# Kernel tuning notes

Hardware: AMD Instinct MI355X
Metric: run time of the kernel (lower is better)

Reference implementation:

```python
import jax, jax.numpy as jnp
import numpy as np

EPS = 1e-5
N, DEG, D, L = 50000, 16, 128, 2  # nodes, max_neighbor, embed_size, gnn_layer


def _log_map_zero(y):
    # Poincare ball log map at origin: atanh(||y||) * y / ||y||, with clamps
    n = jnp.linalg.norm(y, axis=-1, keepdims=True)
    nc = jnp.clip(n, EPS, 1.0 - EPS)
    return y * (jnp.arctanh(nc) / nc)


def _exp_map_zero(v):
    # Poincare ball exp map at origin: tanh(||v||) * v / ||v||
    n = jnp.linalg.norm(v, axis=-1, keepdims=True)
    nc = jnp.maximum(n, EPS)
    return v * (jnp.tanh(nc) / nc)


def setup_inputs() -> dict:
    key = jax.random.key(0)
    k1, k2, k3, k4, k5 = jax.random.split(key, 5)
    node_repr = jax.random.normal(k1, (N, D), jnp.float32) * 0.1
    adj = jax.random.randint(k2, (N, DEG), 0, N)
    weight = jax.random.normal(k3, (N, DEG), jnp.float32)
    mask = jnp.ones((N, 1), jnp.float32)
    # per-relation, per-layer message weights (2 relations: pos / neg edges)
    scale = 1.0 / np.sqrt(D)
    W_pos = jax.random.normal(k4, (L, D, D), jnp.float32) * scale
    W_neg = jax.random.normal(k5, (L, D, D), jnp.float32) * scale
    return {"node_repr": node_repr, "adj": adj, "weight": weight,
            "mask": mask, "W_pos": W_pos, "W_neg": W_neg}


def reference(node_repr, adj, weight, mask, W_pos, W_neg):
    # split_graph_by_negative_edge
    pos_m = (weight > 0).astype(weight.dtype)
    neg_m = (weight < 0).astype(weight.dtype)
    adjs = (adj * pos_m.astype(adj.dtype), adj * neg_m.astype(adj.dtype))
    ws = (weight * pos_m, (-weight) * neg_m)
    Ws = (W_pos, W_neg)

    x = node_repr
    for step in range(L):
        x = (_log_map_zero(x) if step > 0 else x) * mask
        combined = jnp.zeros_like(x)
        for a, w, W in zip(adjs, ws, Ws):
            msg = (x @ W[step]) * mask                    # [N, D]
            nb = msg[a.reshape(-1)].reshape(N, DEG, D)    # neighbor gather
            combined = combined + jnp.sum(w[..., None] * nb, axis=1)
        combined = combined * mask                        # dropout identity (eval)
        x = _exp_map_zero(combined) * mask
        x = jax.nn.relu(x) * mask                         # poincare activation
    return x
```

## Files before the change

### kernel.cpp

```cpp
#include <hip/hip_runtime.h>
#include <math.h>

#define DD 128
#define DEG 16
#define TM 16
#define LDST 136
#define EPSV 1e-5f

typedef _Float16 half4_t __attribute__((ext_vector_type(4)));
typedef _Float16 half8_t __attribute__((ext_vector_type(8)));
typedef float    f32x4   __attribute__((ext_vector_type(4)));

__global__ void prep_x(const float* __restrict__ x, const float* __restrict__ mask,
                       _Float16* __restrict__ x16, int n4)
{
    int i = blockIdx.x * blockDim.x + threadIdx.x;
    if (i >= n4) return;
    float m = mask[i >> 5];
    float m2 = m * m;
    float4 v = ((const float4*)x)[i];
    half4_t h;
    h[0] = (_Float16)(v.x * m2); h[1] = (_Float16)(v.y * m2);
    h[2] = (_Float16)(v.z * m2); h[3] = (_Float16)(v.w * m2);
    ((half4_t*)x16)[i] = h;
}

__global__ void prep_w(const float* __restrict__ Wp, const float* __restrict__ Wn,
                       _Float16* __restrict__ WT)
{
    const int l = blockIdx.x >> 1, rel = blockIdx.x & 1;
    const float* __restrict__ src = (rel ? Wn : Wp) + (size_t)l * DD * DD;
    _Float16* __restrict__ dst = WT + (size_t)blockIdx.x * DD * DD;
    for (int o = threadIdx.x; o < DD * DD; o += blockDim.x) {
        int nn = o >> 7, kk = o & 127;
        dst[o] = (_Float16)src[kk * DD + nn];
    }
}

__global__ __launch_bounds__(256, 6) void fused_layer(
    const _Float16* __restrict__ src16,
    const int*   __restrict__ adj, const float* __restrict__ wgt,
    const float* __restrict__ mask,
    const _Float16* __restrict__ WTp, const _Float16* __restrict__ WTn,
    float* __restrict__ dst_f32, _Float16* __restrict__ dst_f16,
    int n, int apply_logmap)
{
    __shared__ __align__(16) _Float16 aggP[TM][LDST];
    __shared__ __align__(16) _Float16 aggN[TM][LDST];
    __shared__ float partA[4][TM];
    __shared__ float partB[4][TM];

    const int row0   = blockIdx.x * TM;
    const int tid    = threadIdx.x;
    const int lane32 = tid & 31;
    const int hw2    = tid >> 5;

    #pragma unroll
    for (int i = 0; i < 2; ++i) {
        const int r    = hw2 * 2 + i;
        const int node = row0 + r;
        f32x4 aP = {0.f, 0.f, 0.f, 0.f};
        f32x4 aN = {0.f, 0.f, 0.f, 0.f};
        if (node < n) {
            const int*   __restrict__ arow = adj + (size_t)node * DEG;
            const float* __restrict__ wrow = wgt + (size_t)node * DEG;
            #pragma unroll
            for (int b = 0; b < 2; ++b) {
                int4   i0 = ((const int4*)arow)[b * 2 + 0];
                int4   i1 = ((const int4*)arow)[b * 2 + 1];
                float4 w0 = ((const float4*)wrow)[b * 2 + 0];
                float4 w1 = ((const float4*)wrow)[b * 2 + 1];
                const int   idxs[8] = {i0.x, i0.y, i0.z, i0.w, i1.x, i1.y, i1.z, i1.w};
                const float ws[8]   = {w0.x, w0.y, w0.z, w0.w, w1.x, w1.y, w1.z, w1.w};
                half4_t v[8];
                #pragma unroll
                for (int j = 0; j < 8; ++j)
                    v[j] = *(const half4_t*)(src16 + (size_t)idxs[j] * DD + lane32 * 4);
                #pragma unroll
                for (int j = 0; j < 8; ++j) {
                    float wp = fmaxf(ws[j], 0.f);
                    float wn = fmaxf(-ws[j], 0.f);
                    float v0 = (float)v[j][0], v1 = (float)v[j][1];
                    float v2 = (float)v[j][2], v3 = (float)v[j][3];
                    aP[0] += wp * v0; aP[1] += wp * v1; aP[2] += wp * v2; aP[3] += wp * v3;
                    aN[0] += wn * v0; aN[1] += wn * v1; aN[2] += wn * v2; aN[3] += wn * v3;
                }
            }
        }
        half4_t hP, hN;
        hP[0] = (_Float16)aP[0]; hP[1] = (_Float16)aP[1];
        hP[2] = (_Float16)aP[2]; hP[3] = (_Float16)aP[3];
        hN[0] = (_Float16)aN[0]; hN[1] = (_Float16)aN[1];
        hN[2] = (_Float16)aN[2]; hN[3] = (_Float16)aN[3];
        *(half4_t*)&aggP[r][lane32 * 4] = hP;
        *(half4_t*)&aggN[r][lane32 * 4] = hN;
    }
    __syncthreads();

    const int wv2  = tid >> 6;
    const int l64  = tid & 63;
    const int l15  = l64 & 15;
    const int quad = l64 >> 4;

    half8_t aPf[4], aNf[4];
    #pragma unroll
    for (int kb = 0; kb < 4; ++kb) {
        aPf[kb] = *(const half8_t*)&aggP[l15][kb * 32 + quad * 8];
        aNf[kb] = *(const half8_t*)&aggN[l15][kb * 32 + quad * 8];
    }

    f32x4 acc[2];
    acc[0] = (f32x4){0.f, 0.f, 0.f, 0.f};
    acc[1] = (f32x4){0.f, 0.f, 0.f, 0.f};
    #pragma unroll
    for (int t = 0; t < 2; ++t) {
        const int nb = wv2 * 2 + t;
        const _Float16* bp = WTp + (size_t)(nb * 16 + l15) * DD + quad * 8;
        const _Float16* bn = WTn + (size_t)(nb * 16 + l15) * DD + quad * 8;
        #pragma unroll
        for (int kb = 0; kb < 4; ++kb) {
            acc[t] = __builtin_amdgcn_mfma_f32_16x16x32_f16(
                aPf[kb], *(const half8_t*)(bp + kb * 32), acc[t], 0, 0, 0);
            acc[t] = __builtin_amdgcn_mfma_f32_16x16x32_f16(
                aNf[kb], *(const half8_t*)(bn + kb * 32), acc[t], 0, 0, 0);
        }
    }

    float cv0[4], cv1[4], mr[4];
    #pragma unroll
    for (int r = 0; r < 4; ++r) {
        const int rl  = quad * 4 + r;
        const int row = row0 + rl;
        float m = (row < n) ? mask[row] : 0.f;
        mr[r] = m;
        float c0 = acc[0][r] * m, c1 = acc[1][r] * m;
        cv0[r] = c0; cv1[r] = c1;
        float p = c0 * c0 + c1 * c1;
        p += __shfl_xor(p, 1); p += __shfl_xor(p, 2);
        p += __shfl_xor(p, 4); p += __shfl_xor(p, 8);
        if (l15 == 0) partA[wv2][rl] = p;
    }
    __syncthreads();

    float x0[4], x1[4];
    #pragma unroll
    for (int r = 0; r < 4; ++r) {
        const int rl = quad * 4 + r;
        float c2 = partA[0][rl] + partA[1][rl] + partA[2][rl] + partA[3][rl];
        float nc = fmaxf(sqrtf(c2), EPSV);
        float sc = tanhf(nc) / nc;
        float m  = mr[r];
        float t0 = fmaxf(cv0[r] * sc * m, 0.f) * m;
        float t1 = fmaxf(cv1[r] * sc * m, 0.f) * m;
        x0[r] = t0; x1[r] = t1;
        if (apply_logmap) {
            float p = t0 * t0 + t1 * t1;
            p += __shfl_xor(p, 1); p += __shfl_xor(p, 2);
            p += __shfl_xor(p, 4); p += __shfl_xor(p, 8);
            if (l15 == 0) partB[wv2][rl] = p;
        }
    }

    if (apply_logmap) {
        __syncthreads();
        #pragma unroll
        for (int r = 0; r < 4; ++r) {
            const int rl  = quad * 4 + r;
            const int row = row0 + rl;
            if (row >= n) continue;
            float s2  = partB[0][rl] + partB[1][rl] + partB[2][rl] + partB[3][rl];
            float nc2 = fminf(fmaxf(sqrtf(s2), EPSV), 1.f - EPSV);
            float f = (atanhf(nc2) / nc2) * mr[r] * mr[r];
            _Float16* drow = dst_f16 + (size_t)row * DD + wv2 * 32 + l15;
            drow[0]  = (_Float16)(x0[r] * f);
            drow[16] = (_Float16)(x1[r] * f);
        }
    } else {
        #pragma unroll
        for (int r = 0; r < 4; ++r) {
            const int rl  = quad * 4 + r;
            const int row = row0 + rl;
            if (row >= n) continue;
            float* drow = dst_f32 + (size_t)row * DD + wv2 * 32 + l15;
            drow[0]  = x0[r];
            drow[16] = x1[r];
        }
    }
}

extern "C" void kernel_launch(void* const* d_in, const int* in_sizes, int n_in,
                              void* d_out, int out_size, void* d_ws, size_t ws_size,
                              hipStream_t stream)
{
    const float* node_repr = (const float*)d_in[0];
    const int*   adj       = (const int*)  d_in[1];
    const float* weight    = (const float*)d_in[2];
    const float* mask      = (const float*)d_in[3];
    const float* W_pos     = (const float*)d_in[4];
    const float* W_neg     = (const float*)d_in[5];

    const int n = in_sizes[0] / DD;

    _Float16* x16 = (_Float16*)d_ws;
    _Float16* y16 = x16 + (size_t)n * DD;
    _Float16* WT  = y16 + (size_t)n * DD;

    const int n4 = n * DD / 4;
    prep_x<<<(n4 + 255) / 256, 256, 0, stream>>>(node_repr, mask, x16, n4);
    prep_w<<<4, 256, 0, stream>>>(W_pos, W_neg, WT);

    dim3 grid((n + TM - 1) / TM);
    fused_layer<<<grid, 256, 0, stream>>>(x16, adj, weight, mask,
                                          WT + 0 * DD * DD, WT + 1 * DD * DD,
                                          nullptr, y16, n, 1);
    fused_layer<<<grid, 256, 0, stream>>>(y16, adj, weight, mask,
                                          WT + 2 * DD * DD, WT + 3 * DD * DD,
                                          (float*)d_out, nullptr, n, 0);
}
```

Before: 204.7 us.

## Widen neighbor gather to 16-byte loads and merge prep kernels

Each node's aggregation is now handled by 16 threads, each loading all 16 neighbor rows as 8-half (16-byte) vectors, instead of 32 threads doing 4-half loads in two batches. The goal is more bytes per gather instruction and more loads in flight per thread. The two prep kernels are merged into one launch, and the weight transpose is split across 32 blocks to cut launch overhead and serial work. Launch bounds drop from 6 to 4 waves because the 16 outstanding 128-bit loads raise register pressure, which may reduce occupancy.

Result: faster. 188.1 us (-8.1%).

```diff
diff --git a/kernel.cpp b/kernel.cpp
--- a/kernel.cpp
+++ b/kernel.cpp
@@ -11,33 +11,36 @@
 typedef _Float16 half8_t __attribute__((ext_vector_type(8)));
 typedef float    f32x4   __attribute__((ext_vector_type(4)));
 
-__global__ void prep_x(const float* __restrict__ x, const float* __restrict__ mask,
-                       _Float16* __restrict__ x16, int n4)
+__global__ void prep(const float* __restrict__ x, const float* __restrict__ mask,
+                     _Float16* __restrict__ x16, int n4, int xb,
+                     const float* __restrict__ Wp, const float* __restrict__ Wn,
+                     _Float16* __restrict__ WT)
 {
-    int i = blockIdx.x * blockDim.x + threadIdx.x;
-    if (i >= n4) return;
-    float m = mask[i >> 5];
-    float m2 = m * m;
-    float4 v = ((const float4*)x)[i];
-    half4_t h;
-    h[0] = (_Float16)(v.x * m2); h[1] = (_Float16)(v.y * m2);
-    h[2] = (_Float16)(v.z * m2); h[3] = (_Float16)(v.w * m2);
-    ((half4_t*)x16)[i] = h;
+    if ((int)blockIdx.x < xb) {
+        int i = blockIdx.x * blockDim.x + threadIdx.x;
+        if (i >= n4) return;
+        float m = mask[i >> 5];
+        float m2 = m * m;
+        float4 v = ((const float4*)x)[i];
+        half4_t h;
+        h[0] = (_Float16)(v.x * m2); h[1] = (_Float16)(v.y * m2);
+        h[2] = (_Float16)(v.z * m2); h[3] = (_Float16)(v.w * m2);
+        ((half4_t*)x16)[i] = h;
+    } else {
+        int bid   = blockIdx.x - xb;
+        int mat   = bid >> 3;
+        int chunk = bid & 7;
+        int l = mat >> 1, rel = mat & 1;
+        const float* __restrict__ src = (rel ? Wn : Wp) + (size_t)l * DD * DD;
+        _Float16* __restrict__ dst = WT + (size_t)mat * DD * DD;
+        for (int o = chunk * 2048 + threadIdx.x; o < chunk * 2048 + 2048; o += 256) {
+            int nn = o >> 7, kk = o & 127;
+            dst[o] = (_Float16)src[kk * DD + nn];
+        }
+    }
 }
 
-__global__ void prep_w(const float* __restrict__ Wp, const float* __restrict__ Wn,
-                       _Float16* __restrict__ WT)
-{
-    const int l = blockIdx.x >> 1, rel = blockIdx.x & 1;
-    const float* __restrict__ src = (rel ? Wn : Wp) + (size_t)l * DD * DD;
-    _Float16* __restrict__ dst = WT + (size_t)blockIdx.x * DD * DD;
-    for (int o = threadIdx.x; o < DD * DD; o += blockDim.x) {
-        int nn = o >> 7, kk = o & 127;
-        dst[o] = (_Float16)src[kk * DD + nn];
-    }
-}
-
-__global__ __launch_bounds__(256, 6) void fused_layer(
+__global__ __launch_bounds__(256, 4) void fused_layer(
     const _Float16* __restrict__ src16,
     const int*   __restrict__ adj, const float* __restrict__ wgt,
     const float* __restrict__ mask,
@@ -50,51 +53,47 @@
     __shared__ float partA[4][TM];
     __shared__ float partB[4][TM];
 
-    const int row0   = blockIdx.x * TM;
-    const int tid    = threadIdx.x;
-    const int lane32 = tid & 31;
-    const int hw2    = tid >> 5;
-
-    #pragma unroll
-    for (int i = 0; i < 2; ++i) {
-        const int r    = hw2 * 2 + i;
-        const int node = row0 + r;
-        f32x4 aP = {0.f, 0.f, 0.f, 0.f};
-        f32x4 aN = {0.f, 0.f, 0.f, 0.f};
-        if (node < n) {
-            const int*   __restrict__ arow = adj + (size_t)node * DEG;
-            const float* __restrict__ wrow = wgt + (size_t)node * DEG;
+    const int row0 = blockIdx.x * TM;
+    const int tid  = threadIdx.x;
+    const int qw   = tid >> 4;
+    const int l16  = tid & 15;
+
+    float aP[8] = {0.f,0.f,0.f,0.f,0.f,0.f,0.f,0.f};
+    float aN[8] = {0.f,0.f,0.f,0.f,0.f,0.f,0.f,0.f};
+    const int node = row0 + qw;
+    if (node < n) {
+        const int*   __restrict__ arow = adj + (size_t)node * DEG;
+        const float* __restrict__ wrow = wgt + (size_t)node * DEG;
+        int   idxs[16];
+        float ws[16];
+        #pragma unroll
+        for (int b = 0; b < 4; ++b) {
+            int4   ia = ((const int4*)arow)[b];
+            float4 wa = ((const float4*)wrow)[b];
+            idxs[b*4+0] = ia.x; idxs[b*4+1] = ia.y; idxs[b*4+2] = ia.z; idxs[b*4+3] = ia.w;
+            ws[b*4+0] = wa.x; ws[b*4+1] = wa.y; ws[b*4+2] = wa.z; ws[b*4+3] = wa.w;
+        }
+        half8_t v[16];
+        #pragma unroll
+        for (int j = 0; j < 16; ++j)
+            v[j] = *(const half8_t*)(src16 + (size_t)idxs[j] * DD + l16 * 8);
+        #pragma unroll
+        for (int j = 0; j < 16; ++j) {
+            float wp = fmaxf(ws[j], 0.f);
+            float wn = fmaxf(-ws[j], 0.f);
             #pragma unroll
-            for (int b = 0; b < 2; ++b) {
-                int4   i0 = ((const int4*)arow)[b * 2 + 0];
-                int4   i1 = ((const int4*)arow)[b * 2 + 1];
-                float4 w0 = ((const float4*)wrow)[b * 2 + 0];
-                float4 w1 = ((const float4*)wrow)[b * 2 + 1];
-                const int   idxs[8] = {i0.x, i0.y, i0.z, i0.w, i1.x, i1.y, i1.z, i1.w};
-                const float ws[8]   = {w0.x, w0.y, w0.z, w0.w, w1.x, w1.y, w1.z, w1.w};
-                half4_t v[8];
-                #pragma unroll
-                for (int j = 0; j < 8; ++j)
-                    v[j] = *(const half4_t*)(src16 + (size_t)idxs[j] * DD + lane32 * 4);
-                #pragma unroll
-                for (int j = 0; j < 8; ++j) {
-                    float wp = fmaxf(ws[j], 0.f);
-                    float wn = fmaxf(-ws[j], 0.f);
-                    float v0 = (float)v[j][0], v1 = (float)v[j][1];
-                    float v2 = (float)v[j][2], v3 = (float)v[j][3];
-                    aP[0] += wp * v0; aP[1] += wp * v1; aP[2] += wp * v2; aP[3] += wp * v3;
-                    aN[0] += wn * v0; aN[1] += wn * v1; aN[2] += wn * v2; aN[3] += wn * v3;
-                }
+            for (int c = 0; c < 8; ++c) {
+                float f = (float)v[j][c];
+                aP[c] += wp * f;
+                aN[c] += wn * f;
             }
         }
-        half4_t hP, hN;
-        hP[0] = (_Float16)aP[0]; hP[1] = (_Float16)aP[1];
-        hP[2] = (_Float16)aP[2]; hP[3] = (_Float16)aP[3];
-        hN[0] = (_Float16)aN[0]; hN[1] = (_Float16)aN[1];
-        hN[2] = (_Float16)aN[2]; hN[3] = (_Float16)aN[3];
-        *(half4_t*)&aggP[r][lane32 * 4] = hP;
-        *(half4_t*)&aggN[r][lane32 * 4] = hN;
-    }
+    }
+    half8_t hP, hN;
+    #pragma unroll
+    for (int c = 0; c < 8; ++c) { hP[c] = (_Float16)aP[c]; hN[c] = (_Float16)aN[c]; }
+    *(half8_t*)&aggP[qw][l16 * 8] = hP;
+    *(half8_t*)&aggN[qw][l16 * 8] = hN;
     __syncthreads();
 
     const int wv2  = tid >> 6;
@@ -206,8 +205,9 @@
     _Float16* WT  = y16 + (size_t)n * DD;
 
     const int n4 = n * DD / 4;
-    prep_x<<<(n4 + 255) / 256, 256, 0, stream>>>(node_repr, mask, x16, n4);
-    prep_w<<<4, 256, 0, stream>>>(W_pos, W_neg, WT);
+    const int xb = (n4 + 255) / 256;
+    prep<<<xb + 32, 256, 0, stream>>>(node_repr, mask, x16, n4, xb,
+                                      W_pos, W_neg, WT);
 
     dim3 grid((n + TM - 1) / TM);
     fused_layer<<<grid, 256, 0, stream>>>(x16, adj, weight, mask,
```
